# Kernel tuning notes

Measured on AMD Instinct MI355X. Metric: run time of the kernel, lower is better.

## Reference

```python
import jax, jax.numpy as jnp
import numpy as np

B, H, Q, N = 4, 32, 16, 4096
H_KV, D = 8, 128
N_KEEP = 3072
GROUPS = H // H_KV  # num_key_value_groups = 4


def setup_inputs() -> dict:
    key = jax.random.key(0)
    k1, k2, k3, k4 = jax.random.split(key, 4)
    attn_w = jax.random.uniform(k1, (B, H, Q, N), dtype=jnp.float32)
    # normalize to look like softmax output over the kv axis
    attn_w = attn_w / attn_w.sum(-1, keepdims=True)
    v_cache = jax.random.normal(k2, (B, H_KV, N, D), dtype=jnp.float32)
    o_proj_w = jax.random.normal(k3, (H * D, H * D), dtype=jnp.float32) * (1.0 / np.sqrt(H * D))
    keep_idx = jnp.sort(jax.random.randint(k4, (N_KEEP,), 0, N, dtype=jnp.int64))
    return {"attn_w": attn_w, "v_cache": v_cache, "o_proj_w": o_proj_w, "keep_idx": keep_idx}


def reference(attn_w, v_cache, o_proj_w, keep_idx):
    # 1) gather kept KV positions in the attention weights and renormalize
    aw = jnp.take(attn_w, keep_idx, axis=-1)              # [B,H,Q,Nk]
    aw = aw / (aw.sum(-1, keepdims=True) + 1e-6)
    # 2) gather kept V entries and repeat_kv across query-head groups
    v_new = jnp.take(v_cache, keep_idx, axis=2)           # [B,H_kv,Nk,D]
    v_all = jnp.repeat(v_new, GROUPS, axis=1)             # [B,H,Nk,D]
    # 3) recompute context and output projection
    ctx = jnp.einsum('bhqn,bhnd->bhqd', aw, v_all)        # [B,H,Q,D]
    ctx = ctx.transpose(0, 2, 1, 3).reshape(B, Q, H * D)  # [B,Q,H*D]
    out = ctx @ o_proj_w.T                                # nn.Linear: x @ W^T
    return out, aw
```

## Files before the change

kernel.cpp:

```cpp
#include <hip/hip_runtime.h>
#include <hip/hip_bf16.h>

#define BB   4
#define HH   32
#define QQ   16
#define NN   4096
#define HKV  8
#define DD   128
#define NK   3072
#define GRP  4

typedef __attribute__((ext_vector_type(8))) short bf16x8;
typedef __attribute__((ext_vector_type(4))) float f32x4;

__device__ __forceinline__ unsigned int pack_bf16(float lo, float hi) {
    union { unsigned int u; __hip_bfloat16 h[2]; } p;
    p.h[0] = __float2bfloat16(lo);
    p.h[1] = __float2bfloat16(hi);
    return p.u;
}

__global__ __launch_bounds__(256)
void k1_gather_norm(const float* __restrict__ attn_w,
                    const int* __restrict__ keep_idx,
                    float* __restrict__ aw_out,
                    __hip_bfloat16* __restrict__ aw16)
{
    const int row = blockIdx.x;
    const float* src = attn_w + (size_t)row * NN;
    float* dst = aw_out + (size_t)row * NK;
    unsigned int* dst16 = reinterpret_cast<unsigned int*>(aw16 + (size_t)row * NK);

    __shared__ float vals[NK];
    __shared__ float red[256];

    float s = 0.f;
    for (int k = threadIdx.x; k < NK; k += 256) {
        float v = src[keep_idx[k]];
        vals[k] = v;
        s += v;
    }
    red[threadIdx.x] = s;
    __syncthreads();
    for (int st = 128; st > 0; st >>= 1) {
        if (threadIdx.x < st) red[threadIdx.x] += red[threadIdx.x + st];
        __syncthreads();
    }
    const float inv = 1.0f / (red[0] + 1e-6f);
    for (int k = threadIdx.x * 2; k < NK; k += 512) {
        float a = vals[k] * inv;
        float b = vals[k + 1] * inv;
        *reinterpret_cast<float2*>(&dst[k]) = make_float2(a, b);
        dst16[k >> 1] = pack_bf16(a, b);
    }
}

#define SPLITK2 16
#define KPB2    (NK / SPLITK2)
#define KCH     64

__global__ __launch_bounds__(512, 4)
void k2_ctx(const __hip_bfloat16* __restrict__ aw16,
            const float* __restrict__ v_cache,
            const int* __restrict__ keep_idx,
            __hip_bfloat16* __restrict__ partial)
{
    const int bid = blockIdx.x;
    const int ks  = bid & 15;
    const int hkv = (bid >> 4) & 7;
    const int b   = bid >> 7;
    const int tid = threadIdx.x;
    const int lane = tid & 63;
    const int w    = tid >> 6;
    const int mw   = w & 3;
    const int nh   = w >> 2;
    const int fr   = lane & 15;
    const int kg   = lane >> 4;

    __shared__ unsigned short Vt[128 * 64];
    __shared__ int idxs[KCH];

    const int k0 = ks * KPB2;
    const unsigned short* arow = reinterpret_cast<const unsigned short*>(aw16)
        + (size_t)((b * HH + hkv * GRP + mw) * QQ + fr) * NK + k0;
    const float* vb = v_cache + (size_t)(b * HKV + hkv) * NN * DD;

    f32x4 acc[4];
#pragma unroll
    for (int nt = 0; nt < 4; ++nt) acc[nt] = (f32x4){0.f, 0.f, 0.f, 0.f};

    const int sd  = tid & 127;
    const int sc0 = tid >> 7;

    for (int c = 0; c < KPB2; c += KCH) {
        __syncthreads();
        if (tid < KCH) idxs[tid] = keep_idx[k0 + c + tid];
        __syncthreads();

#pragma unroll
        for (int p = 0; p < 2; ++p) {
            const int cs = sc0 + 4 * p;
            float v[8];
#pragma unroll
            for (int e = 0; e < 8; ++e)
                v[e] = vb[(size_t)idxs[8 * cs + e] * DD + sd];
            uint4 pk;
            pk.x = pack_bf16(v[0], v[1]);
            pk.y = pack_bf16(v[2], v[3]);
            pk.z = pack_bf16(v[4], v[5]);
            pk.w = pack_bf16(v[6], v[7]);
            const int us = sd * 64 + ((cs ^ (sd & 7)) << 3);
            *reinterpret_cast<uint4*>(&Vt[us]) = pk;
        }
        __syncthreads();

#pragma unroll
        for (int kc = 0; kc < 2; ++kc) {
            bf16x8 af = *reinterpret_cast<const bf16x8*>(arow + c + kc * 32 + kg * 8);
            const int cs = kc * 4 + kg;
            const int xr = (cs ^ (fr & 7)) << 3;
#pragma unroll
            for (int nt = 0; nt < 4; ++nt) {
                const int d  = (nh * 4 + nt) * 16 + fr;
                const int us = d * 64 + xr;
                bf16x8 bf = *reinterpret_cast<const bf16x8*>(&Vt[us]);
                acc[nt] = __builtin_amdgcn_mfma_f32_16x16x32_bf16(af, bf, acc[nt], 0, 0, 0);
            }
        }
    }

    __hip_bfloat16* pb = partial + (size_t)bid * (64 * DD);
#pragma unroll
    for (int nt = 0; nt < 4; ++nt) {
#pragma unroll
        for (int reg = 0; reg < 4; ++reg) {
            const int row = mw * 16 + kg * 4 + reg;
            pb[row * DD + (nh * 4 + nt) * 16 + fr] = __float2bfloat16(acc[nt][reg]);
        }
    }
}

__global__ __launch_bounds__(256)
void k3_reduce(const __hip_bfloat16* __restrict__ partial,
               __hip_bfloat16* __restrict__ ctxb)
{
    const int flat = blockIdx.x * 256 + threadIdx.x;
    const int bq = flat >> 12;
    const int i  = flat & 4095;
    const int b = bq >> 4, q = bq & 15;
    const int h = i >> 7,  d = i & 127;
    const int hkv = h >> 2, g = h & 3;
    const int r = g * 16 + q;

    const __hip_bfloat16* p = partial
        + (size_t)((b * 8 + hkv) * SPLITK2) * (64 * DD) + r * DD + d;
    float s = 0.f;
#pragma unroll
    for (int ss = 0; ss < SPLITK2; ++ss)
        s += __bfloat162float(p[(size_t)ss * (64 * DD)]);
    ctxb[flat] = __float2bfloat16(s);
}

#define K4SPLIT 8
#define K4LEN   (4096 / K4SPLIT)
#define KC4     128
#define LPAD    136

__global__ __launch_bounds__(256, 4)
void k4_gemm(const __hip_bfloat16* __restrict__ ctxb,
             const float* __restrict__ W,
             __hip_bfloat16* __restrict__ pout)
{
    const int nt  = blockIdx.x >> 3;
    const int ks  = blockIdx.x & 7;
    const int tid = threadIdx.x;
    const int lane = tid & 63;
    const int w    = tid >> 6;

    __shared__ unsigned short Al[64][LPAD];
    __shared__ unsigned short Bl[32][LPAD];

    f32x4 acc0 = {0.f, 0.f, 0.f, 0.f};
    f32x4 acc1 = {0.f, 0.f, 0.f, 0.f};

    const unsigned short* ctxu = reinterpret_cast<const unsigned short*>(ctxb);
    const int kbase = ks * K4LEN;
    const int fr = lane & 15;
    const int kg = lane >> 4;

    for (int ch = 0; ch < K4LEN / KC4; ++ch) {
        const int kb = kbase + ch * KC4;
        __syncthreads();

        {
            const int cc = tid & 15;
            const int r0 = tid >> 4;
#pragma unroll
            for (int p = 0; p < 4; ++p) {
                const int r = r0 + p * 16;
                float4 v = *reinterpret_cast<const float4*>(
                    ctxu + (size_t)r * 4096 + kb + cc * 8);
                *reinterpret_cast<float4*>(&Al[r][cc * 8]) = v;
            }
        }
        {
            const int cc = tid & 31;
            const int r0 = tid >> 5;
#pragma unroll
            for (int p = 0; p < 4; ++p) {
                const int r = r0 + p * 8;
                float4 v = *reinterpret_cast<const float4*>(
                    W + (size_t)(nt * 32 + r) * 4096 + kb + cc * 4);
                union { ushort4 u; __hip_bfloat16 h[4]; } pk;
                pk.h[0] = __float2bfloat16(v.x);
                pk.h[1] = __float2bfloat16(v.y);
                pk.h[2] = __float2bfloat16(v.z);
                pk.h[3] = __float2bfloat16(v.w);
                *reinterpret_cast<ushort4*>(&Bl[r][cc * 4]) = pk.u;
            }
        }
        __syncthreads();

#pragma unroll
        for (int kst = 0; kst < KC4 / 32; ++kst) {
            const int ko = kst * 32 + kg * 8;
            bf16x8 a  = *reinterpret_cast<const bf16x8*>(&Al[w * 16 + fr][ko]);
            bf16x8 b0 = *reinterpret_cast<const bf16x8*>(&Bl[fr][ko]);
            bf16x8 b1 = *reinterpret_cast<const bf16x8*>(&Bl[16 + fr][ko]);
            acc0 = __builtin_amdgcn_mfma_f32_16x16x32_bf16(a, b0, acc0, 0, 0, 0);
            acc1 = __builtin_amdgcn_mfma_f32_16x16x32_bf16(a, b1, acc1, 0, 0, 0);
        }
    }

    __hip_bfloat16* pb = pout + (size_t)ks * (64 * 4096);
#pragma unroll
    for (int reg = 0; reg < 4; ++reg) {
        const int row = w * 16 + kg * 4 + reg;
        pb[(size_t)row * 4096 + nt * 32 + fr]      = __float2bfloat16(acc0[reg]);
        pb[(size_t)row * 4096 + nt * 32 + 16 + fr] = __float2bfloat16(acc1[reg]);
    }
}

__global__ __launch_bounds__(256)
void k5_out(const __hip_bfloat16* __restrict__ pout, float* __restrict__ out)
{
    const int flat = blockIdx.x * 256 + threadIdx.x;
    float s = 0.f;
#pragma unroll
    for (int ss = 0; ss < K4SPLIT; ++ss)
        s += __bfloat162float(pout[(size_t)ss * (64 * 4096) + flat]);
    out[flat] = s;
}

extern "C" void kernel_launch(void* const* d_in, const int* in_sizes, int n_in,
                              void* d_out, int out_size, void* d_ws, size_t ws_size,
                              hipStream_t stream)
{
    const float* attn_w  = (const float*)d_in[0];
    const float* v_cache = (const float*)d_in[1];
    const float* o_proj  = (const float*)d_in[2];
    const int*   keep_idx = (const int*)d_in[3];

    float* out    = (float*)d_out;
    float* aw_out = (float*)d_out + 262144;

    __hip_bfloat16* partial2 = (__hip_bfloat16*)d_ws;
    __hip_bfloat16* ctxb = (__hip_bfloat16*)((char*)d_ws + (size_t)8 * 1024 * 1024);
    __hip_bfloat16* aw16 = (__hip_bfloat16*)((char*)d_ws + (size_t)9 * 1024 * 1024);
    __hip_bfloat16* pout = (__hip_bfloat16*)d_ws;

    k1_gather_norm<<<BB * HH * QQ, 256, 0, stream>>>(attn_w, keep_idx, aw_out, aw16);
    k2_ctx<<<BB * HKV * SPLITK2, 512, 0, stream>>>(aw16, v_cache, keep_idx, partial2);
    k3_reduce<<<(64 * 4096) / 256, 256, 0, stream>>>(partial2, ctxb);
    k4_gemm<<<128 * K4SPLIT, 256, 0, stream>>>(ctxb, o_proj, pout);
    k5_out<<<(64 * 4096) / 256, 256, 0, stream>>>(pout, out);
}
```

Before: 48.47 us.

## Replace split-K partials with in-block K-half reductions, drop reduce kernels

The ctx kernel now splits work over 16-wide D slices instead of 16 K-splits. Two wave groups each cover half of the kept positions and combine through shared memory, so ctx is written directly and the separate reduce kernel goes away. The output GEMM likewise uses 16-column tiles with an in-block two-way K split and writes fp32 output directly, removing the split-K partial buffer and the final sum kernel. This cuts two launches and the partial-buffer traffic. In exchange each block does a long serial K loop, and in the ctx kernel every block re-gathers V rows with narrower per-thread loads.

```diff
diff --git a/kernel.cpp b/kernel.cpp
--- a/kernel.cpp
+++ b/kernel.cpp
@@ -55,62 +55,59 @@
     }
 }
 
-#define SPLITK2 16
-#define KPB2    (NK / SPLITK2)
-#define KCH     64
-
-__global__ __launch_bounds__(512, 4)
+#define KH2  1536
+#define KCH  64
+
+__global__ __launch_bounds__(512, 2)
 void k2_ctx(const __hip_bfloat16* __restrict__ aw16,
             const float* __restrict__ v_cache,
             const int* __restrict__ keep_idx,
-            __hip_bfloat16* __restrict__ partial)
+            __hip_bfloat16* __restrict__ ctxb)
 {
     const int bid = blockIdx.x;
-    const int ks  = bid & 15;
-    const int hkv = (bid >> 4) & 7;
-    const int b   = bid >> 7;
+    const int ds  = bid & 7;
+    const int hkv = (bid >> 3) & 7;
+    const int b   = bid >> 6;
     const int tid = threadIdx.x;
     const int lane = tid & 63;
     const int w    = tid >> 6;
     const int mw   = w & 3;
-    const int nh   = w >> 2;
+    const int kh   = w >> 2;
     const int fr   = lane & 15;
     const int kg   = lane >> 4;
 
-    __shared__ unsigned short Vt[128 * 64];
-    __shared__ int idxs[KCH];
-
-    const int k0 = ks * KPB2;
+    __shared__ unsigned short Vt[2 * 16 * 64];
+    __shared__ int idxs[2][KCH];
+    __shared__ float Rt[4][16][16];
+
     const unsigned short* arow = reinterpret_cast<const unsigned short*>(aw16)
-        + (size_t)((b * HH + hkv * GRP + mw) * QQ + fr) * NK + k0;
-    const float* vb = v_cache + (size_t)(b * HKV + hkv) * NN * DD;
-
-    f32x4 acc[4];
-#pragma unroll
-    for (int nt = 0; nt < 4; ++nt) acc[nt] = (f32x4){0.f, 0.f, 0.f, 0.f};
-
-    const int sd  = tid & 127;
-    const int sc0 = tid >> 7;
-
-    for (int c = 0; c < KPB2; c += KCH) {
-        __syncthreads();
-        if (tid < KCH) idxs[tid] = keep_idx[k0 + c + tid];
-        __syncthreads();
-
-#pragma unroll
-        for (int p = 0; p < 2; ++p) {
-            const int cs = sc0 + 4 * p;
-            float v[8];
-#pragma unroll
-            for (int e = 0; e < 8; ++e)
-                v[e] = vb[(size_t)idxs[8 * cs + e] * DD + sd];
-            uint4 pk;
-            pk.x = pack_bf16(v[0], v[1]);
-            pk.y = pack_bf16(v[2], v[3]);
-            pk.z = pack_bf16(v[4], v[5]);
-            pk.w = pack_bf16(v[6], v[7]);
-            const int us = sd * 64 + ((cs ^ (sd & 7)) << 3);
-            *reinterpret_cast<uint4*>(&Vt[us]) = pk;
+        + (size_t)((b * HH + hkv * GRP + mw) * QQ + fr) * NK + kh * KH2;
+    const float* vb = v_cache + (size_t)(b * HKV + hkv) * NN * DD + ds * 16;
+
+    f32x4 acc = {0.f, 0.f, 0.f, 0.f};
+
+    const int sd   = tid & 15;
+    const int scs2 = (tid >> 4) & 15;
+    const int skh  = tid >> 8;
+
+    for (int c = 0; c < KH2; c += KCH) {
+        __syncthreads();
+        if (tid < 128)
+            idxs[tid >> 6][tid & 63] = keep_idx[(tid >> 6) * KH2 + c + (tid & 63)];
+        __syncthreads();
+
+        {
+            const int kbase = scs2 * 4;
+            float v0 = vb[(size_t)idxs[skh][kbase + 0] * DD + sd];
+            float v1 = vb[(size_t)idxs[skh][kbase + 1] * DD + sd];
+            float v2 = vb[(size_t)idxs[skh][kbase + 2] * DD + sd];
+            float v3 = vb[(size_t)idxs[skh][kbase + 3] * DD + sd];
+            uint2 pk;
+            pk.x = pack_bf16(v0, v1);
+            pk.y = pack_bf16(v2, v3);
+            const int us = skh * 1024 + sd * 64
+                         + (((scs2 >> 1) ^ (sd & 7)) << 3) + ((scs2 & 1) << 2);
+            *reinterpret_cast<uint2*>(&Vt[us]) = pk;
         }
         __syncthreads();
 
@@ -118,138 +115,109 @@
         for (int kc = 0; kc < 2; ++kc) {
             bf16x8 af = *reinterpret_cast<const bf16x8*>(arow + c + kc * 32 + kg * 8);
             const int cs = kc * 4 + kg;
-            const int xr = (cs ^ (fr & 7)) << 3;
-#pragma unroll
-            for (int nt = 0; nt < 4; ++nt) {
-                const int d  = (nh * 4 + nt) * 16 + fr;
-                const int us = d * 64 + xr;
-                bf16x8 bf = *reinterpret_cast<const bf16x8*>(&Vt[us]);
-                acc[nt] = __builtin_amdgcn_mfma_f32_16x16x32_bf16(af, bf, acc[nt], 0, 0, 0);
-            }
-        }
-    }
-
-    __hip_bfloat16* pb = partial + (size_t)bid * (64 * DD);
-#pragma unroll
-    for (int nt = 0; nt < 4; ++nt) {
+            const int us = kh * 1024 + fr * 64 + ((cs ^ (fr & 7)) << 3);
+            bf16x8 bf = *reinterpret_cast<const bf16x8*>(&Vt[us]);
+            acc = __builtin_amdgcn_mfma_f32_16x16x32_bf16(af, bf, acc, 0, 0, 0);
+        }
+    }
+
+    __syncthreads();
+    if (kh == 1) {
+#pragma unroll
+        for (int reg = 0; reg < 4; ++reg)
+            Rt[mw][kg * 4 + reg][fr] = acc[reg];
+    }
+    __syncthreads();
+    if (kh == 0) {
 #pragma unroll
         for (int reg = 0; reg < 4; ++reg) {
-            const int row = mw * 16 + kg * 4 + reg;
-            pb[row * DD + (nh * 4 + nt) * 16 + fr] = __float2bfloat16(acc[nt][reg]);
-        }
-    }
-}
-
-__global__ __launch_bounds__(256)
-void k3_reduce(const __hip_bfloat16* __restrict__ partial,
-               __hip_bfloat16* __restrict__ ctxb)
-{
-    const int flat = blockIdx.x * 256 + threadIdx.x;
-    const int bq = flat >> 12;
-    const int i  = flat & 4095;
-    const int b = bq >> 4, q = bq & 15;
-    const int h = i >> 7,  d = i & 127;
-    const int hkv = h >> 2, g = h & 3;
-    const int r = g * 16 + q;
-
-    const __hip_bfloat16* p = partial
-        + (size_t)((b * 8 + hkv) * SPLITK2) * (64 * DD) + r * DD + d;
-    float s = 0.f;
-#pragma unroll
-    for (int ss = 0; ss < SPLITK2; ++ss)
-        s += __bfloat162float(p[(size_t)ss * (64 * DD)]);
-    ctxb[flat] = __float2bfloat16(s);
-}
-
-#define K4SPLIT 8
-#define K4LEN   (4096 / K4SPLIT)
-#define KC4     128
-#define LPAD    136
-
-__global__ __launch_bounds__(256, 4)
+            const float f = acc[reg] + Rt[mw][kg * 4 + reg][fr];
+            const int q  = kg * 4 + reg;
+            const int bq = b * QQ + q;
+            const int i  = (hkv * GRP + mw) * DD + ds * 16 + fr;
+            ctxb[(size_t)bq * 4096 + i] = __float2bfloat16(f);
+        }
+    }
+}
+
+#define KH4  2048
+#define KC4  128
+#define LPAD 136
+
+__global__ __launch_bounds__(512, 2)
 void k4_gemm(const __hip_bfloat16* __restrict__ ctxb,
              const float* __restrict__ W,
-             __hip_bfloat16* __restrict__ pout)
-{
-    const int nt  = blockIdx.x >> 3;
-    const int ks  = blockIdx.x & 7;
+             float* __restrict__ out)
+{
+    const int nt  = blockIdx.x;
     const int tid = threadIdx.x;
     const int lane = tid & 63;
     const int w    = tid >> 6;
-
-    __shared__ unsigned short Al[64][LPAD];
-    __shared__ unsigned short Bl[32][LPAD];
-
-    f32x4 acc0 = {0.f, 0.f, 0.f, 0.f};
-    f32x4 acc1 = {0.f, 0.f, 0.f, 0.f};
+    const int mw   = w & 3;
+    const int kh   = w >> 2;
+    const int fr   = lane & 15;
+    const int kg   = lane >> 4;
+
+    __shared__ unsigned short Al[2][64][LPAD];
+    __shared__ unsigned short Bl[2][16][LPAD];
+    __shared__ float Rt[4][16][16];
 
     const unsigned short* ctxu = reinterpret_cast<const unsigned short*>(ctxb);
-    const int kbase = ks * K4LEN;
-    const int fr = lane & 15;
-    const int kg = lane >> 4;
-
-    for (int ch = 0; ch < K4LEN / KC4; ++ch) {
-        const int kb = kbase + ch * KC4;
-        __syncthreads();
-
-        {
-            const int cc = tid & 15;
-            const int r0 = tid >> 4;
-#pragma unroll
-            for (int p = 0; p < 4; ++p) {
-                const int r = r0 + p * 16;
-                float4 v = *reinterpret_cast<const float4*>(
-                    ctxu + (size_t)r * 4096 + kb + cc * 8);
-                *reinterpret_cast<float4*>(&Al[r][cc * 8]) = v;
-            }
-        }
-        {
-            const int cc = tid & 31;
-            const int r0 = tid >> 5;
-#pragma unroll
-            for (int p = 0; p < 4; ++p) {
-                const int r = r0 + p * 8;
-                float4 v = *reinterpret_cast<const float4*>(
-                    W + (size_t)(nt * 32 + r) * 4096 + kb + cc * 4);
-                union { ushort4 u; __hip_bfloat16 h[4]; } pk;
-                pk.h[0] = __float2bfloat16(v.x);
-                pk.h[1] = __float2bfloat16(v.y);
-                pk.h[2] = __float2bfloat16(v.z);
-                pk.h[3] = __float2bfloat16(v.w);
-                *reinterpret_cast<ushort4*>(&Bl[r][cc * 4]) = pk.u;
-            }
-        }
-        __syncthreads();
-
-#pragma unroll
-        for (int kst = 0; kst < KC4 / 32; ++kst) {
-            const int ko = kst * 32 + kg * 8;
-            bf16x8 a  = *reinterpret_cast<const bf16x8*>(&Al[w * 16 + fr][ko]);
-            bf16x8 b0 = *reinterpret_cast<const bf16x8*>(&Bl[fr][ko]);
-            bf16x8 b1 = *reinterpret_cast<const bf16x8*>(&Bl[16 + fr][ko]);
-            acc0 = __builtin_amdgcn_mfma_f32_16x16x32_bf16(a, b0, acc0, 0, 0, 0);
-            acc1 = __builtin_amdgcn_mfma_f32_16x16x32_bf16(a, b1, acc1, 0, 0, 0);
-        }
-    }
-
-    __hip_bfloat16* pb = pout + (size_t)ks * (64 * 4096);
-#pragma unroll
-    for (int reg = 0; reg < 4; ++reg) {
-        const int row = w * 16 + kg * 4 + reg;
-        pb[(size_t)row * 4096 + nt * 32 + fr]      = __float2bfloat16(acc0[reg]);
-        pb[(size_t)row * 4096 + nt * 32 + 16 + fr] = __float2bfloat16(acc1[reg]);
-    }
-}
-
-__global__ __launch_bounds__(256)
-void k5_out(const __hip_bfloat16* __restrict__ pout, float* __restrict__ out)
-{
-    const int flat = blockIdx.x * 256 + threadIdx.x;
-    float s = 0.f;
-#pragma unroll
-    for (int ss = 0; ss < K4SPLIT; ++ss)
-        s += __bfloat162float(pout[(size_t)ss * (64 * 4096) + flat]);
-    out[flat] = s;
+    f32x4 acc = {0.f, 0.f, 0.f, 0.f};
+
+    for (int i = 0; i < 16; ++i) {
+        __syncthreads();
+
+#pragma unroll
+        for (int p = 0; p < 4; ++p) {
+            const int u  = tid + 512 * p;
+            const int c8 = u & 15;
+            const int r  = (u >> 4) & 63;
+            const int ah = u >> 10;
+            *reinterpret_cast<float4*>(&Al[ah][r][c8 * 8]) =
+                *reinterpret_cast<const float4*>(
+                    ctxu + (size_t)r * 4096 + ah * KH4 + i * KC4 + c8 * 8);
+        }
+#pragma unroll
+        for (int p = 0; p < 2; ++p) {
+            const int u  = tid + 512 * p;
+            const int cc = u & 31;
+            const int r  = (u >> 5) & 15;
+            const int bh = u >> 9;
+            float4 v = *reinterpret_cast<const float4*>(
+                W + (size_t)(nt * 16 + r) * 4096 + bh * KH4 + i * KC4 + cc * 4);
+            union { ushort4 u4; __hip_bfloat16 h[4]; } pk;
+            pk.h[0] = __float2bfloat16(v.x);
+            pk.h[1] = __float2bfloat16(v.y);
+            pk.h[2] = __float2bfloat16(v.z);
+            pk.h[3] = __float2bfloat16(v.w);
+            *reinterpret_cast<ushort4*>(&Bl[bh][r][cc * 4]) = pk.u4;
+        }
+        __syncthreads();
+
+#pragma unroll
+        for (int kc = 0; kc < 4; ++kc) {
+            const int ko = kc * 32 + kg * 8;
+            bf16x8 a  = *reinterpret_cast<const bf16x8*>(&Al[kh][mw * 16 + fr][ko]);
+            bf16x8 bv = *reinterpret_cast<const bf16x8*>(&Bl[kh][fr][ko]);
+            acc = __builtin_amdgcn_mfma_f32_16x16x32_bf16(a, bv, acc, 0, 0, 0);
+        }
+    }
+
+    __syncthreads();
+    if (kh == 1) {
+#pragma unroll
+        for (int reg = 0; reg < 4; ++reg)
+            Rt[mw][kg * 4 + reg][fr] = acc[reg];
+    }
+    __syncthreads();
+    if (kh == 0) {
+#pragma unroll
+        for (int reg = 0; reg < 4; ++reg) {
+            const int bq = mw * 16 + kg * 4 + reg;
+            out[(size_t)bq * 4096 + nt * 16 + fr] = acc[reg] + Rt[mw][kg * 4 + reg][fr];
+        }
+    }
 }
 
 extern "C" void kernel_launch(void* const* d_in, const int* in_sizes, int n_in,
@@ -264,14 +232,10 @@
     float* out    = (float*)d_out;
     float* aw_out = (float*)d_out + 262144;
 
-    __hip_bfloat16* partial2 = (__hip_bfloat16*)d_ws;
-    __hip_bfloat16* ctxb = (__hip_bfloat16*)((char*)d_ws + (size_t)8 * 1024 * 1024);
-    __hip_bfloat16* aw16 = (__hip_bfloat16*)((char*)d_ws + (size_t)9 * 1024 * 1024);
-    __hip_bfloat16* pout = (__hip_bfloat16*)d_ws;
+    __hip_bfloat16* ctxb = (__hip_bfloat16*)d_ws;
+    __hip_bfloat16* aw16 = (__hip_bfloat16*)((char*)d_ws + (size_t)1 * 1024 * 1024);
 
     k1_gather_norm<<<BB * HH * QQ, 256, 0, stream>>>(attn_w, keep_idx, aw_out, aw16);
-    k2_ctx<<<BB * HKV * SPLITK2, 512, 0, stream>>>(aw16, v_cache, keep_idx, partial2);
-    k3_reduce<<<(64 * 4096) / 256, 256, 0, stream>>>(partial2, ctxb);
-    k4_gemm<<<128 * K4SPLIT, 256, 0, stream>>>(ctxb, o_proj, pout);
-    k5_out<<<(64 * 4096) / 256, 256, 0, stream>>>(pout, out);
-}
+    k2_ctx<<<256, 512, 0, stream>>>(aw16, v_cache, keep_idx, ctxb);
+    k4_gemm<<<256, 512, 0, stream>>>(ctxb, o_proj, out);
+}
```

Result: slower. 80.77 us (+66.6%).

## Replace split-K partial buffers and reduce kernels with float atomics

Applied to the files above, without the earlier changes.

Both split-K stages now accumulate directly into fp32 buffers using unsafe atomic adds, replacing the separate bf16 partial-buffer writes and the two reduction kernels (k3, k5). The zeroing of the context and output buffers is folded into the first gather kernel. The GEMM now loads fp32 context and converts it to bf16 in LDS. This removes two launches and the partial-buffer traffic, at the cost of atomic contention, nondeterministic summation order and more bytes read for the context.

```diff
diff --git a/kernel.cpp b/kernel.cpp
--- a/kernel.cpp
+++ b/kernel.cpp
@@ -20,16 +20,28 @@
     return p.u;
 }
 
+__device__ __forceinline__ void atomAddF32(float* p, float v) {
+    unsafeAtomicAdd(p, v);
+}
+
 __global__ __launch_bounds__(256)
 void k1_gather_norm(const float* __restrict__ attn_w,
                     const int* __restrict__ keep_idx,
                     float* __restrict__ aw_out,
-                    __hip_bfloat16* __restrict__ aw16)
+                    __hip_bfloat16* __restrict__ aw16,
+                    float* __restrict__ ctxf,
+                    float* __restrict__ out)
 {
     const int row = blockIdx.x;
     const float* src = attn_w + (size_t)row * NN;
     float* dst = aw_out + (size_t)row * NK;
     unsigned int* dst16 = reinterpret_cast<unsigned int*>(aw16 + (size_t)row * NK);
+
+    {
+        const int flat = blockIdx.x * 256 + threadIdx.x;
+        if (flat < 262144) ctxf[flat] = 0.f;
+        else               out[flat - 262144] = 0.f;
+    }
 
     __shared__ float vals[NK];
     __shared__ float red[256];
@@ -63,7 +75,7 @@
 void k2_ctx(const __hip_bfloat16* __restrict__ aw16,
             const float* __restrict__ v_cache,
             const int* __restrict__ keep_idx,
-            __hip_bfloat16* __restrict__ partial)
+            float* __restrict__ ctxf)
 {
     const int bid = blockIdx.x;
     const int ks  = bid & 15;
@@ -129,36 +141,16 @@
         }
     }
 
-    __hip_bfloat16* pb = partial + (size_t)bid * (64 * DD);
 #pragma unroll
     for (int nt = 0; nt < 4; ++nt) {
 #pragma unroll
         for (int reg = 0; reg < 4; ++reg) {
-            const int row = mw * 16 + kg * 4 + reg;
-            pb[row * DD + (nh * 4 + nt) * 16 + fr] = __float2bfloat16(acc[nt][reg]);
-        }
-    }
-}
-
-__global__ __launch_bounds__(256)
-void k3_reduce(const __hip_bfloat16* __restrict__ partial,
-               __hip_bfloat16* __restrict__ ctxb)
-{
-    const int flat = blockIdx.x * 256 + threadIdx.x;
-    const int bq = flat >> 12;
-    const int i  = flat & 4095;
-    const int b = bq >> 4, q = bq & 15;
-    const int h = i >> 7,  d = i & 127;
-    const int hkv = h >> 2, g = h & 3;
-    const int r = g * 16 + q;
-
-    const __hip_bfloat16* p = partial
-        + (size_t)((b * 8 + hkv) * SPLITK2) * (64 * DD) + r * DD + d;
-    float s = 0.f;
-#pragma unroll
-    for (int ss = 0; ss < SPLITK2; ++ss)
-        s += __bfloat162float(p[(size_t)ss * (64 * DD)]);
-    ctxb[flat] = __float2bfloat16(s);
+            const int q  = kg * 4 + reg;
+            const int d  = (nh * 4 + nt) * 16 + fr;
+            atomAddF32(&ctxf[(size_t)(b * QQ + q) * 4096
+                             + (hkv * GRP + mw) * DD + d], acc[nt][reg]);
+        }
+    }
 }
 
 #define K4SPLIT 8
@@ -167,9 +159,9 @@
 #define LPAD    136
 
 __global__ __launch_bounds__(256, 4)
-void k4_gemm(const __hip_bfloat16* __restrict__ ctxb,
+void k4_gemm(const float* __restrict__ ctxf,
              const float* __restrict__ W,
-             __hip_bfloat16* __restrict__ pout)
+             float* __restrict__ out)
 {
     const int nt  = blockIdx.x >> 3;
     const int ks  = blockIdx.x & 7;
@@ -183,7 +175,6 @@
     f32x4 acc0 = {0.f, 0.f, 0.f, 0.f};
     f32x4 acc1 = {0.f, 0.f, 0.f, 0.f};
 
-    const unsigned short* ctxu = reinterpret_cast<const unsigned short*>(ctxb);
     const int kbase = ks * K4LEN;
     const int fr = lane & 15;
     const int kg = lane >> 4;
@@ -192,32 +183,33 @@
         const int kb = kbase + ch * KC4;
         __syncthreads();
 
-        {
-            const int cc = tid & 15;
-            const int r0 = tid >> 4;
-#pragma unroll
-            for (int p = 0; p < 4; ++p) {
-                const int r = r0 + p * 16;
-                float4 v = *reinterpret_cast<const float4*>(
-                    ctxu + (size_t)r * 4096 + kb + cc * 8);
-                *reinterpret_cast<float4*>(&Al[r][cc * 8]) = v;
-            }
-        }
-        {
-            const int cc = tid & 31;
-            const int r0 = tid >> 5;
-#pragma unroll
-            for (int p = 0; p < 4; ++p) {
-                const int r = r0 + p * 8;
-                float4 v = *reinterpret_cast<const float4*>(
-                    W + (size_t)(nt * 32 + r) * 4096 + kb + cc * 4);
-                union { ushort4 u; __hip_bfloat16 h[4]; } pk;
-                pk.h[0] = __float2bfloat16(v.x);
-                pk.h[1] = __float2bfloat16(v.y);
-                pk.h[2] = __float2bfloat16(v.z);
-                pk.h[3] = __float2bfloat16(v.w);
-                *reinterpret_cast<ushort4*>(&Bl[r][cc * 4]) = pk.u;
-            }
+#pragma unroll
+        for (int p = 0; p < 8; ++p) {
+            const int u  = tid + 256 * p;
+            const int cc = u & 31;
+            const int r  = u >> 5;
+            float4 v = *reinterpret_cast<const float4*>(
+                ctxf + (size_t)r * 4096 + kb + cc * 4);
+            union { ushort4 u4; __hip_bfloat16 h[4]; } pk;
+            pk.h[0] = __float2bfloat16(v.x);
+            pk.h[1] = __float2bfloat16(v.y);
+            pk.h[2] = __float2bfloat16(v.z);
+            pk.h[3] = __float2bfloat16(v.w);
+            *reinterpret_cast<ushort4*>(&Al[r][cc * 4]) = pk.u4;
+        }
+#pragma unroll
+        for (int p = 0; p < 4; ++p) {
+            const int u  = tid + 256 * p;
+            const int cc = u & 31;
+            const int r  = u >> 5;
+            float4 v = *reinterpret_cast<const float4*>(
+                W + (size_t)(nt * 32 + r) * 4096 + kb + cc * 4);
+            union { ushort4 u4; __hip_bfloat16 h[4]; } pk;
+            pk.h[0] = __float2bfloat16(v.x);
+            pk.h[1] = __float2bfloat16(v.y);
+            pk.h[2] = __float2bfloat16(v.z);
+            pk.h[3] = __float2bfloat16(v.w);
+            *reinterpret_cast<ushort4*>(&Bl[r][cc * 4]) = pk.u4;
         }
         __syncthreads();
 
@@ -232,24 +224,12 @@
         }
     }
 
-    __hip_bfloat16* pb = pout + (size_t)ks * (64 * 4096);
 #pragma unroll
     for (int reg = 0; reg < 4; ++reg) {
         const int row = w * 16 + kg * 4 + reg;
-        pb[(size_t)row * 4096 + nt * 32 + fr]      = __float2bfloat16(acc0[reg]);
-        pb[(size_t)row * 4096 + nt * 32 + 16 + fr] = __float2bfloat16(acc1[reg]);
-    }
-}
-
-__global__ __launch_bounds__(256)
-void k5_out(const __hip_bfloat16* __restrict__ pout, float* __restrict__ out)
-{
-    const int flat = blockIdx.x * 256 + threadIdx.x;
-    float s = 0.f;
-#pragma unroll
-    for (int ss = 0; ss < K4SPLIT; ++ss)
-        s += __bfloat162float(pout[(size_t)ss * (64 * 4096) + flat]);
-    out[flat] = s;
+        atomAddF32(&out[(size_t)row * 4096 + nt * 32 + fr],      acc0[reg]);
+        atomAddF32(&out[(size_t)row * 4096 + nt * 32 + 16 + fr], acc1[reg]);
+    }
 }
 
 extern "C" void kernel_launch(void* const* d_in, const int* in_sizes, int n_in,
@@ -264,14 +244,11 @@
     float* out    = (float*)d_out;
     float* aw_out = (float*)d_out + 262144;
 
-    __hip_bfloat16* partial2 = (__hip_bfloat16*)d_ws;
-    __hip_bfloat16* ctxb = (__hip_bfloat16*)((char*)d_ws + (size_t)8 * 1024 * 1024);
-    __hip_bfloat16* aw16 = (__hip_bfloat16*)((char*)d_ws + (size_t)9 * 1024 * 1024);
-    __hip_bfloat16* pout = (__hip_bfloat16*)d_ws;
-
-    k1_gather_norm<<<BB * HH * QQ, 256, 0, stream>>>(attn_w, keep_idx, aw_out, aw16);
-    k2_ctx<<<BB * HKV * SPLITK2, 512, 0, stream>>>(aw16, v_cache, keep_idx, partial2);
-    k3_reduce<<<(64 * 4096) / 256, 256, 0, stream>>>(partial2, ctxb);
-    k4_gemm<<<128 * K4SPLIT, 256, 0, stream>>>(ctxb, o_proj, pout);
-    k5_out<<<(64 * 4096) / 256, 256, 0, stream>>>(pout, out);
-}
+    float* ctxf = (float*)d_ws;
+    __hip_bfloat16* aw16 = (__hip_bfloat16*)((char*)d_ws + (size_t)1 * 1024 * 1024);
+
+    k1_gather_norm<<<BB * HH * QQ, 256, 0, stream>>>(attn_w, keep_idx, aw_out,
+                                                     aw16, ctxf, out);
+    k2_ctx<<<BB * HKV * SPLITK2, 512, 0, stream>>>(aw16, v_cache, keep_idx, ctxf);
+    k4_gemm<<<128 * K4SPLIT, 256, 0, stream>>>(ctxf, o_proj, out);
+}
```

After: 60.06 us. 1.24x slower.
